# Kernel optimization log

Measured on AMD Instinct MI355X. Metric: run time of the kernel, lower is better.

The kernel has to match this reference:

```python
import jax, jax.numpy as jnp
import numpy as np

EPS = 1e-5

def _layernorm(h, g, b):
    m = jnp.mean(h, axis=-1, keepdims=True)
    v = jnp.mean((h - m) ** 2, axis=-1, keepdims=True)
    return (h - m) * jax.lax.rsqrt(v + EPS) * g + b

def setup_inputs() -> dict:
    B, N, D, H, C = 16, 4096, 1024, 512, 2
    key = jax.random.key(0)
    ks = jax.random.split(key, 16)
    def lin(k, fan_in, shape):
        return jax.random.normal(k, shape, dtype=jnp.float32) / np.sqrt(fan_in)
    return {
        "x":   jax.random.normal(ks[0], (B, N, D), dtype=jnp.float32),
        "W1":  lin(ks[1], D, (D, H)),  "b1": jnp.zeros((H,), jnp.float32),
        "g1":  jnp.ones((H,), jnp.float32), "beta1": jnp.zeros((H,), jnp.float32),
        "W2":  lin(ks[2], H, (H, H)),  "b2": jnp.zeros((H,), jnp.float32),
        "g2":  jnp.ones((H,), jnp.float32), "beta2": jnp.zeros((H,), jnp.float32),
        "Wa1": lin(ks[3], H, (H, H)),  "ba1": jnp.zeros((H,), jnp.float32),
        "wa2": lin(ks[4], H, (H, 1)),  "ba2": jnp.zeros((1,), jnp.float32),
        "Wc1": lin(ks[5], H, (H, H)),  "bc1": jnp.zeros((H,), jnp.float32),
        "Wc2": lin(ks[6], H, (H, C)),  "bc2": jnp.zeros((C,), jnp.float32),
    }

def reference(x, W1, b1, g1, beta1, W2, b2, g2, beta2,
              Wa1, ba1, wa2, ba2, Wc1, bc1, Wc2, bc2):
    # Feature extractor: Linear -> LayerNorm -> ReLU (x2); dropout is identity (eval)
    h = jax.nn.relu(_layernorm(jnp.einsum('bnd,dh->bnh', x, W1) + b1, g1, beta1))
    h = jax.nn.relu(_layernorm(jnp.einsum('bnh,hk->bnk', h, W2) + b2, g2, beta2))
    # Attention: Linear -> Tanh -> Linear(->1), softmax over instances (per bag)
    scores = jnp.tanh(jnp.einsum('bnh,hk->bnk', h, Wa1) + ba1) @ wa2 + ba2  # [B,N,1]
    attn = jax.nn.softmax(scores, axis=1)                                   # [B,N,1]
    pooled = jnp.sum(h * attn, axis=1)                                      # [B,H]
    # Classifier (no sample_source path): Linear -> ReLU -> Linear
    logits = jax.nn.relu(pooled @ Wc1 + bc1) @ Wc2 + bc2                    # [B,C]
    return logits
```

## Files before the change

### kernel.cpp

```cpp
#include <hip/hip_runtime.h>
#include <hip/hip_bf16.h>


#define MTOT   65536
#define DDIM   1024
#define HDIM   512
#define NBAG   16
#define NINST  4096

typedef __attribute__((ext_vector_type(8))) short bf16x8;
typedef __attribute__((ext_vector_type(4))) float f32x4;

__device__ __forceinline__ unsigned short f2bf(float f) {
  __hip_bfloat16 h = __float2bfloat16(f);
  unsigned short u;
  __builtin_memcpy(&u, &h, 2);
  return u;
}
__device__ __forceinline__ float bf2f(unsigned short u) {
  unsigned int x = ((unsigned int)u) << 16;
  float f;
  __builtin_memcpy(&f, &x, 4);
  return f;
}

__device__ __forceinline__ void gload16(const void* g, void* l) {
  __builtin_amdgcn_global_load_lds(
      (const __attribute__((address_space(1))) unsigned int*)g,
      (__attribute__((address_space(3))) unsigned int*)l, 16, 0, 0);
}

__device__ __forceinline__ bf16x8 pack8(float4 a, float4 b) {
  bf16x8 r;
  r[0] = (short)f2bf(a.x); r[1] = (short)f2bf(a.y);
  r[2] = (short)f2bf(a.z); r[3] = (short)f2bf(a.w);
  r[4] = (short)f2bf(b.x); r[5] = (short)f2bf(b.y);
  r[6] = (short)f2bf(b.z); r[7] = (short)f2bf(b.w);
  return r;
}

__global__ void transpose_cast(const float* __restrict__ src,
                               __hip_bfloat16* __restrict__ dst,
                               int R, int C) {
  __shared__ float t[32][33];
  const int c0 = blockIdx.x * 32, r0 = blockIdx.y * 32;
  const int tx = threadIdx.x, ty = threadIdx.y;
#pragma unroll
  for (int i = 0; i < 32; i += 8)
    t[ty + i][tx] = src[(size_t)(r0 + ty + i) * C + c0 + tx];
  __syncthreads();
#pragma unroll
  for (int i = 0; i < 32; i += 8)
    dst[(size_t)(c0 + ty + i) * R + r0 + tx] = __float2bfloat16(t[tx][ty + i]);
}

#define BM 128
#define BK 64
#define NW 8

template <int KD, bool AF32, int MODE>
__global__ __launch_bounds__(512, 2)
void gemm_fused(const void* Ap, const __hip_bfloat16* __restrict__ BT,
                const float* __restrict__ bias, const float* __restrict__ gg,
                const float* __restrict__ bb, const float* __restrict__ wa2,
                const float* __restrict__ ba2, __hip_bfloat16* __restrict__ outh,
                float* __restrict__ outs) {
  __shared__ __hip_bfloat16 At[2][BM * BK];
  __shared__ __hip_bfloat16 Bt[HDIM * BK];
  __shared__ float redS[BM][4];
  __shared__ float redQ[BM][4];
  __shared__ float muL[BM];
  __shared__ float rsL[BM];

  const int tid  = threadIdx.x;
  const int lane = tid & 63;
  const int w    = tid >> 6;
  const int wm   = w >> 2;
  const int wn   = w & 3;
  const int l16  = lane & 15;
  const int lg   = lane >> 4;
  const size_t row0 = (size_t)blockIdx.x * BM;

  const int sr = tid >> 3;
  const int sp = tid & 7;

  f32x4 acc[4][8];
#pragma unroll
  for (int i = 0; i < 4; i++)
#pragma unroll
    for (int j = 0; j < 8; j++) acc[i][j] = (f32x4){0.f, 0.f, 0.f, 0.f};

  const int NT = KD / BK;
  const __hip_bfloat16* Abf = (const __hip_bfloat16*)Ap;
  const float* Af32 = (const float*)Ap;

  auto stageB = [&](int kb) {
#pragma unroll
    for (int i = 0; i < 8; i++) {
      const int row = i * 64 + sr;
      const int slog = sp ^ (row & 7);
      gload16(BT + (size_t)row * KD + kb + slog * 8, &Bt[row * BK + sp * 8]);
    }
  };
  auto stageA_lds = [&](int kb, int buf) {
#pragma unroll
    for (int j = 0; j < 2; j++) {
      const int row = j * 64 + sr;
      const int slog = sp ^ (row & 7);
      gload16(Abf + (row0 + row) * KD + kb + slog * 8,
              &At[buf][row * BK + sp * 8]);
    }
  };

  float4 fa[2][2];
  auto loadA_f32 = [&](int kb) {
#pragma unroll
    for (int j = 0; j < 2; j++) {
      const int row = j * 64 + sr;
      const int slog = sp ^ (row & 7);
      const float* gp = Af32 + (row0 + row) * KD + kb + slog * 8;
      fa[j][0] = *reinterpret_cast<const float4*>(gp);
      fa[j][1] = *reinterpret_cast<const float4*>(gp + 4);
    }
  };
  auto writeA_f32 = [&](int buf) {
#pragma unroll
    for (int j = 0; j < 2; j++) {
      const int row = j * 64 + sr;
      *reinterpret_cast<bf16x8*>(&At[buf][row * BK + sp * 8]) =
          pack8(fa[j][0], fa[j][1]);
    }
  };

  if (AF32) {
    loadA_f32(0);
    writeA_f32(0);
  } else {
    stageA_lds(0, 0);
  }
  stageB(0);
  __syncthreads();

  int cur = 0;
  for (int t = 0; t < NT; ++t) {
    const int kb_next = (t + 1) * BK;
    if (t + 1 < NT) {
      if (AF32) loadA_f32(kb_next);
      else      stageA_lds(kb_next, cur ^ 1);
    }
#pragma unroll
    for (int h = 0; h < 2; ++h) {
      bf16x8 af[4], bfr[8];
#pragma unroll
      for (int fm = 0; fm < 4; fm++) {
        const int row = wm * 64 + fm * 16 + l16;
        const int s = (h * 4 + lg) ^ (row & 7);
        af[fm] = *reinterpret_cast<const bf16x8*>(&At[cur][row * BK + s * 8]);
      }
#pragma unroll
      for (int fn = 0; fn < 8; fn++) {
        const int row = wn * 128 + fn * 16 + l16;
        const int s = (h * 4 + lg) ^ (row & 7);
        bfr[fn] = *reinterpret_cast<const bf16x8*>(&Bt[row * BK + s * 8]);
      }
#pragma unroll
      for (int fm = 0; fm < 4; fm++)
#pragma unroll
        for (int fn = 0; fn < 8; fn++)
          acc[fm][fn] = __builtin_amdgcn_mfma_f32_16x16x32_bf16(
              af[fm], bfr[fn], acc[fm][fn], 0, 0, 0);
    }
    __syncthreads();
    if (t + 1 < NT) {
      if (AF32) writeA_f32(cur ^ 1);
      stageB(kb_next);
    }
    __syncthreads();
    cur ^= 1;
  }

  float biasv[8];
#pragma unroll
  for (int fn = 0; fn < 8; fn++) biasv[fn] = bias[wn * 128 + fn * 16 + l16];

  if (MODE == 0) {
    float gv[8], bv[8];
#pragma unroll
    for (int fn = 0; fn < 8; fn++) {
      const int col = wn * 128 + fn * 16 + l16;
      gv[fn] = gg[col];
      bv[fn] = bb[col];
    }
#pragma unroll
    for (int fm = 0; fm < 4; fm++)
#pragma unroll
      for (int r = 0; r < 4; r++) {
        float s1 = 0.f, s2 = 0.f;
#pragma unroll
        for (int fn = 0; fn < 8; fn++) {
          const float v = acc[fm][fn][r] + biasv[fn];
          s1 += v;
          s2 += v * v;
        }
#pragma unroll
        for (int m = 1; m < 16; m <<= 1) {
          s1 += __shfl_xor(s1, m);
          s2 += __shfl_xor(s2, m);
        }
        if (l16 == 0) {
          const int rl = wm * 64 + fm * 16 + lg * 4 + r;
          redS[rl][wn] = s1;
          redQ[rl][wn] = s2;
        }
      }
    __syncthreads();
    if (tid < BM) {
      const float S = redS[tid][0] + redS[tid][1] + redS[tid][2] + redS[tid][3];
      const float Q = redQ[tid][0] + redQ[tid][1] + redQ[tid][2] + redQ[tid][3];
      const float mean = S * (1.f / 512.f);
      const float var = Q * (1.f / 512.f) - mean * mean;
      muL[tid] = mean;
      rsL[tid] = rsqrtf(var + 1e-5f);
    }
    __syncthreads();
#pragma unroll
    for (int fm = 0; fm < 4; fm++)
#pragma unroll
      for (int r = 0; r < 4; r++) {
        const int rl = wm * 64 + fm * 16 + lg * 4 + r;
        const float mu = muL[rl], rs = rsL[rl];
#pragma unroll
        for (int fn = 0; fn < 8; fn++) {
          const float v = acc[fm][fn][r] + biasv[fn];
          float y = (v - mu) * rs * gv[fn] + bv[fn];
          y = fmaxf(y, 0.f);
          outh[(row0 + rl) * HDIM + wn * 128 + fn * 16 + l16] =
              __float2bfloat16(y);
        }
      }
  } else {
    float wv[8];
#pragma unroll
    for (int fn = 0; fn < 8; fn++) wv[fn] = wa2[wn * 128 + fn * 16 + l16];
#pragma unroll
    for (int fm = 0; fm < 4; fm++)
#pragma unroll
      for (int r = 0; r < 4; r++) {
        float s = 0.f;
#pragma unroll
        for (int fn = 0; fn < 8; fn++) {
          const float v = acc[fm][fn][r] + biasv[fn];
          s += tanhf(v) * wv[fn];
        }
#pragma unroll
        for (int m = 1; m < 16; m <<= 1) s += __shfl_xor(s, m);
        if (l16 == 0) redS[wm * 64 + fm * 16 + lg * 4 + r][wn] = s;
      }
    __syncthreads();
    if (tid < BM) {
      outs[row0 + tid] =
          redS[tid][0] + redS[tid][1] + redS[tid][2] + redS[tid][3] + ba2[0];
    }
  }
}

__global__ void softmax_bag(const float* __restrict__ sc, float* __restrict__ at) {
  const int b = blockIdx.x;
  const int tid = threadIdx.x;
  const int lane = tid & 63, w = tid >> 6;
  const float* s = sc + (size_t)b * NINST;
  float v[16];
  float mx = -1e30f;
#pragma unroll
  for (int i = 0; i < 16; i++) {
    v[i] = s[tid + i * 256];
    mx = fmaxf(mx, v[i]);
  }
#pragma unroll
  for (int off = 32; off; off >>= 1) mx = fmaxf(mx, __shfl_xor(mx, off));
  __shared__ float red[4];
  if (lane == 0) red[w] = mx;
  __syncthreads();
  mx = fmaxf(fmaxf(red[0], red[1]), fmaxf(red[2], red[3]));
  float sum = 0.f;
#pragma unroll
  for (int i = 0; i < 16; i++) {
    v[i] = expf(v[i] - mx);
    sum += v[i];
  }
#pragma unroll
  for (int off = 32; off; off >>= 1) sum += __shfl_xor(sum, off);
  __shared__ float red2[4];
  if (lane == 0) red2[w] = sum;
  __syncthreads();
  sum = red2[0] + red2[1] + red2[2] + red2[3];
  const float inv = 1.f / sum;
#pragma unroll
  for (int i = 0; i < 16; i++) at[(size_t)b * NINST + tid + i * 256] = v[i] * inv;
}

__global__ void pooled_partial(const __hip_bfloat16* __restrict__ h2,
                               const float* __restrict__ at,
                               float* __restrict__ part) {
  const int bid = blockIdx.x;
  const int b = bid >> 5, cc = (bid >> 3) & 3, nch = bid & 7;
  const int tid = threadIdx.x;
  const int c4 = (tid & 31) * 4, sub = tid >> 5;
  const int n0 = nch * 512;
  const size_t base = (size_t)b * NINST;
  float a0 = 0.f, a1 = 0.f, a2 = 0.f, a3 = 0.f;
  for (int n = n0 + sub; n < n0 + 512; n += 8) {
    const float a = at[base + n];
    const ushort4 u = *reinterpret_cast<const ushort4*>(
        &h2[(base + n) * HDIM + cc * 128 + c4]);
    a0 += a * bf2f(u.x);
    a1 += a * bf2f(u.y);
    a2 += a * bf2f(u.z);
    a3 += a * bf2f(u.w);
  }
  __shared__ float pb[8][128];
  pb[sub][c4 + 0] = a0;
  pb[sub][c4 + 1] = a1;
  pb[sub][c4 + 2] = a2;
  pb[sub][c4 + 3] = a3;
  __syncthreads();
  if (tid < 128) {
    float s = 0.f;
#pragma unroll
    for (int j = 0; j < 8; j++) s += pb[j][tid];
    part[(size_t)nch * 8192 + b * 512 + cc * 128 + tid] = s;
  }
}

__global__ void pooled_reduce(const float* __restrict__ part,
                              float* __restrict__ pooled) {
  const int i = blockIdx.x * 256 + threadIdx.x;
  float s = 0.f;
#pragma unroll
  for (int j = 0; j < 8; j++) s += part[(size_t)j * 8192 + i];
  pooled[i] = s;
}

__global__ void classifier(const float* __restrict__ pooled,
                           const float* __restrict__ Wc1,
                           const float* __restrict__ bc1,
                           const float* __restrict__ Wc2,
                           const float* __restrict__ bc2,
                           float* __restrict__ out) {
  __shared__ float P[NBAG][512];
  __shared__ float Rb[NBAG][512];
  const int tid = threadIdx.x;
#pragma unroll
  for (int i = 0; i < NBAG; i++) P[i][tid] = pooled[i * 512 + tid];
  __syncthreads();
  float r[NBAG];
#pragma unroll
  for (int i = 0; i < NBAG; i++) r[i] = 0.f;
  for (int k = 0; k < 512; k++) {
    const float wv = Wc1[k * 512 + tid];
#pragma unroll
    for (int i = 0; i < NBAG; i++) r[i] += P[i][k] * wv;
  }
#pragma unroll
  for (int i = 0; i < NBAG; i++) Rb[i][tid] = fmaxf(r[i] + bc1[tid], 0.f);
  __syncthreads();
  if (tid < 32) {
    const int i = tid >> 1, c = tid & 1;
    float s = bc2[c];
    for (int k = 0; k < 512; k++) s += Rb[i][k] * Wc2[k * 2 + c];
    out[i * 2 + c] = s;
  }
}

extern "C" void kernel_launch(void* const* d_in, const int* in_sizes, int n_in,
                              void* d_out, int out_size, void* d_ws,
                              size_t ws_size, hipStream_t stream) {
  const float* x   = (const float*)d_in[0];
  const float* W1  = (const float*)d_in[1];
  const float* b1  = (const float*)d_in[2];
  const float* g1  = (const float*)d_in[3];
  const float* be1 = (const float*)d_in[4];
  const float* W2  = (const float*)d_in[5];
  const float* b2  = (const float*)d_in[6];
  const float* g2  = (const float*)d_in[7];
  const float* be2 = (const float*)d_in[8];
  const float* Wa1 = (const float*)d_in[9];
  const float* ba1 = (const float*)d_in[10];
  const float* wa2 = (const float*)d_in[11];
  const float* ba2 = (const float*)d_in[12];
  const float* Wc1 = (const float*)d_in[13];
  const float* bc1 = (const float*)d_in[14];
  const float* Wc2 = (const float*)d_in[15];
  const float* bc2 = (const float*)d_in[16];
  float* out = (float*)d_out;

  char* ws = (char*)d_ws;
  __hip_bfloat16* W1T = (__hip_bfloat16*)(ws + 0);
  __hip_bfloat16* W2T = (__hip_bfloat16*)(ws + 1048576);
  __hip_bfloat16* WaT = (__hip_bfloat16*)(ws + 1572864);
  float* scores = (float*)(ws + 2097152);
  float* attn   = (float*)(ws + 2359296);
  float* part   = (float*)(ws + 2621440);
  float* pooled = (float*)(ws + 2883584);
  __hip_bfloat16* hbuf = (__hip_bfloat16*)(ws + 4194304);

  transpose_cast<<<dim3(16, 32), dim3(32, 8), 0, stream>>>(W1, W1T, DDIM, HDIM);
  transpose_cast<<<dim3(16, 16), dim3(32, 8), 0, stream>>>(W2, W2T, HDIM, HDIM);
  transpose_cast<<<dim3(16, 16), dim3(32, 8), 0, stream>>>(Wa1, WaT, HDIM, HDIM);

  gemm_fused<DDIM, true, 0><<<MTOT / BM, 512, 0, stream>>>(
      x, W1T, b1, g1, be1, nullptr, nullptr, hbuf, nullptr);
  gemm_fused<HDIM, false, 0><<<MTOT / BM, 512, 0, stream>>>(
      hbuf, W2T, b2, g2, be2, nullptr, nullptr, hbuf, nullptr);
  gemm_fused<HDIM, false, 1><<<MTOT / BM, 512, 0, stream>>>(
      hbuf, WaT, ba1, nullptr, nullptr, wa2, ba2, nullptr, scores);

  softmax_bag<<<NBAG, 256, 0, stream>>>(scores, attn);
  pooled_partial<<<512, 256, 0, stream>>>(hbuf, attn, part);
  pooled_reduce<<<32, 256, 0, stream>>>(part, pooled);
  classifier<<<1, 512, 0, stream>>>(pooled, Wc1, bc1, Wc2, bc2, out);
}
```

Baseline: 386.5 us.

## Deepen GEMM main loop into multi-stage async pipeline with split MFMA phases

Reworks the fused GEMM main loop to use BK=32 with a 4-deep B buffer ring and double-buffered A, issuing global loads two steps ahead. Explicit vmcnt/lgkmcnt waits, split-phase barriers, sched_barrier and setprio interleave the loads with two halves of the MFMA work. The goal is to hide global and LDS load latency behind tensor-core math instead of stalling on a full __syncthreads each k-step. In exchange it adds more barriers per k-step and fragile hand-counted waitcnt values, which could cause races or stalls if the counts are wrong.

```diff
diff --git a/kernel.cpp b/kernel.cpp
--- a/kernel.cpp
+++ b/kernel.cpp
@@ -39,6 +39,9 @@
   return r;
 }
 
+#define VMW(N) asm volatile("s_waitcnt vmcnt(" #N ")" ::: "memory")
+#define LKW0   asm volatile("s_waitcnt lgkmcnt(0)" ::: "memory")
+
 __global__ void transpose_cast(const float* __restrict__ src,
                                __hip_bfloat16* __restrict__ dst,
                                int R, int C) {
@@ -55,8 +58,7 @@
 }
 
 #define BM 128
-#define BK 64
-#define NW 8
+#define BK 32
 
 template <int KD, bool AF32, int MODE>
 __global__ __launch_bounds__(512, 2)
@@ -66,7 +68,7 @@
                 const float* __restrict__ ba2, __hip_bfloat16* __restrict__ outh,
                 float* __restrict__ outs) {
   __shared__ __hip_bfloat16 At[2][BM * BK];
-  __shared__ __hip_bfloat16 Bt[HDIM * BK];
+  __shared__ __hip_bfloat16 Bt[4][HDIM * BK];
   __shared__ float redS[BM][4];
   __shared__ float redQ[BM][4];
   __shared__ float muL[BM];
@@ -81,103 +83,123 @@
   const int lg   = lane >> 4;
   const size_t row0 = (size_t)blockIdx.x * BM;
 
-  const int sr = tid >> 3;
-  const int sp = tid & 7;
-
-  f32x4 acc[4][8];
-#pragma unroll
-  for (int i = 0; i < 4; i++)
-#pragma unroll
-    for (int j = 0; j < 8; j++) acc[i][j] = (f32x4){0.f, 0.f, 0.f, 0.f};
-
-  const int NT = KD / BK;
+  const int sr = tid >> 2;
+  const int sp = tid & 3;
+  const int slogA = sp ^ (sr & 3);
+
+  constexpr int NT = KD / BK;
   const __hip_bfloat16* Abf = (const __hip_bfloat16*)Ap;
   const float* Af32 = (const float*)Ap;
 
-  auto stageB = [&](int kb) {
-#pragma unroll
-    for (int i = 0; i < 8; i++) {
-      const int row = i * 64 + sr;
-      const int slog = sp ^ (row & 7);
-      gload16(BT + (size_t)row * KD + kb + slog * 8, &Bt[row * BK + sp * 8]);
+  f32x4 acc[4][8];
+#pragma unroll
+  for (int i = 0; i < 4; i++)
+#pragma unroll
+    for (int j = 0; j < 8; j++) acc[i][j] = (f32x4){0.f, 0.f, 0.f, 0.f};
+
+  auto issueB2 = [&](int kb, int buf, int half) {
+#pragma unroll
+    for (int i = 0; i < 2; i++) {
+      const int row = (half * 2 + i) * 128 + sr;
+      const int slog = sp ^ (row & 3);
+      gload16(BT + (size_t)row * KD + kb + slog * 8, &Bt[buf][row * BK + sp * 8]);
     }
   };
-  auto stageA_lds = [&](int kb, int buf) {
-#pragma unroll
-    for (int j = 0; j < 2; j++) {
-      const int row = j * 64 + sr;
-      const int slog = sp ^ (row & 7);
-      gload16(Abf + (row0 + row) * KD + kb + slog * 8,
-              &At[buf][row * BK + sp * 8]);
-    }
+  auto issueA_g = [&](int kb, int buf) {
+    gload16(Abf + (row0 + sr) * KD + kb + slogA * 8, &At[buf][sr * BK + sp * 8]);
   };
 
-  float4 fa[2][2];
-  auto loadA_f32 = [&](int kb) {
-#pragma unroll
-    for (int j = 0; j < 2; j++) {
-      const int row = j * 64 + sr;
-      const int slog = sp ^ (row & 7);
-      const float* gp = Af32 + (row0 + row) * KD + kb + slog * 8;
-      fa[j][0] = *reinterpret_cast<const float4*>(gp);
-      fa[j][1] = *reinterpret_cast<const float4*>(gp + 4);
-    }
-  };
-  auto writeA_f32 = [&](int buf) {
-#pragma unroll
-    for (int j = 0; j < 2; j++) {
-      const int row = j * 64 + sr;
-      *reinterpret_cast<bf16x8*>(&At[buf][row * BK + sp * 8]) =
-          pack8(fa[j][0], fa[j][1]);
-    }
-  };
-
-  if (AF32) {
-    loadA_f32(0);
-    writeA_f32(0);
+  float4 fr0a, fr0b, fr1a, fr1b;
+#define LOADA(FR, TT)                                                          \
+  { const float* gp_ = Af32 + (row0 + sr) * KD + (TT) * BK + slogA * 8;        \
+    FR##a = *reinterpret_cast<const float4*>(gp_);                             \
+    FR##b = *reinterpret_cast<const float4*>(gp_ + 4); }
+#define CVTA(FR, BUF)                                                          \
+  { *reinterpret_cast<bf16x8*>(&At[(BUF)][sr * BK + sp * 8]) =                 \
+        pack8(FR##a, FR##b); }
+
+#define MFMA_HALF(FN0)                                                         \
+  _Pragma("unroll") for (int fm = 0; fm < 4; fm++)                             \
+  _Pragma("unroll") for (int fn = (FN0); fn < (FN0) + 4; fn++)                 \
+      acc[fm][fn] = __builtin_amdgcn_mfma_f32_16x16x32_bf16(                   \
+          af[fm], bfr[fn], acc[fm][fn], 0, 0, 0);
+
+  if constexpr (AF32) {
+    LOADA(fr0, 0); VMW(0); CVTA(fr0, 0);
+    issueB2(0, 0, 0); issueB2(0, 0, 1);
+    LOADA(fr1, 1);
+    issueB2(BK, 1, 0); issueB2(BK, 1, 1);
+    LKW0;
+    __builtin_amdgcn_s_barrier();
   } else {
-    stageA_lds(0, 0);
-  }
-  stageB(0);
-  __syncthreads();
-
-  int cur = 0;
-  for (int t = 0; t < NT; ++t) {
-    const int kb_next = (t + 1) * BK;
-    if (t + 1 < NT) {
-      if (AF32) loadA_f32(kb_next);
-      else      stageA_lds(kb_next, cur ^ 1);
-    }
-#pragma unroll
-    for (int h = 0; h < 2; ++h) {
-      bf16x8 af[4], bfr[8];
-#pragma unroll
-      for (int fm = 0; fm < 4; fm++) {
-        const int row = wm * 64 + fm * 16 + l16;
-        const int s = (h * 4 + lg) ^ (row & 7);
-        af[fm] = *reinterpret_cast<const bf16x8*>(&At[cur][row * BK + s * 8]);
-      }
-#pragma unroll
-      for (int fn = 0; fn < 8; fn++) {
-        const int row = wn * 128 + fn * 16 + l16;
-        const int s = (h * 4 + lg) ^ (row & 7);
-        bfr[fn] = *reinterpret_cast<const bf16x8*>(&Bt[row * BK + s * 8]);
-      }
-#pragma unroll
-      for (int fm = 0; fm < 4; fm++)
-#pragma unroll
-        for (int fn = 0; fn < 8; fn++)
-          acc[fm][fn] = __builtin_amdgcn_mfma_f32_16x16x32_bf16(
-              af[fm], bfr[fn], acc[fm][fn], 0, 0, 0);
-    }
-    __syncthreads();
-    if (t + 1 < NT) {
-      if (AF32) writeA_f32(cur ^ 1);
-      stageB(kb_next);
-    }
-    __syncthreads();
-    cur ^= 1;
-  }
+    issueA_g(0, 0);
+    issueB2(0, 0, 0); issueB2(0, 0, 1);
+    issueB2(BK, 1, 0); issueB2(BK, 1, 1);
+    __builtin_amdgcn_s_barrier();
+  }
+
+#define GSTEP(J)                                                               \
+  {                                                                            \
+    const int t = tb + (J);                                                    \
+    if constexpr (AF32) { VMW(6); } else { VMW(4); }                           \
+    bf16x8 af[4], bfr[8];                                                      \
+    _Pragma("unroll") for (int fm = 0; fm < 4; fm++) {                         \
+      const int row = wm * 64 + fm * 16 + l16;                                 \
+      af[fm] = *reinterpret_cast<const bf16x8*>(                               \
+          &At[(J) & 1][row * BK + (lg ^ (row & 3)) * 8]);                      \
+    }                                                                          \
+    _Pragma("unroll") for (int fn = 0; fn < 4; fn++) {                         \
+      const int row = wn * 128 + fn * 16 + l16;                                \
+      bfr[fn] = *reinterpret_cast<const bf16x8*>(                              \
+          &Bt[(J) & 3][row * BK + (lg ^ (row & 3)) * 8]);                      \
+    }                                                                          \
+    if constexpr (AF32) {                                                      \
+      if (t + 2 < NT) {                                                        \
+        if constexpr (((J) & 1) == 0) { LOADA(fr0, t + 2); }                   \
+        else                          { LOADA(fr1, t + 2); }                   \
+      }                                                                        \
+    } else {                                                                   \
+      if (t + 1 < NT) issueA_g((t + 1) * BK, ((J) + 1) & 1);                   \
+    }                                                                          \
+    if (t + 2 < NT) issueB2((t + 2) * BK, ((J) + 2) & 3, 0);                   \
+    __builtin_amdgcn_s_barrier();                                              \
+    LKW0; __builtin_amdgcn_sched_barrier(0);                                   \
+    __builtin_amdgcn_s_setprio(1);                                             \
+    MFMA_HALF(0)                                                               \
+    __builtin_amdgcn_s_setprio(0);                                             \
+    __builtin_amdgcn_s_barrier();                                              \
+    _Pragma("unroll") for (int fn = 4; fn < 8; fn++) {                         \
+      const int row = wn * 128 + fn * 16 + l16;                                \
+      bfr[fn] = *reinterpret_cast<const bf16x8*>(                              \
+          &Bt[(J) & 3][row * BK + (lg ^ (row & 3)) * 8]);                      \
+    }                                                                          \
+    if (t + 2 < NT) issueB2((t + 2) * BK, ((J) + 2) & 3, 1);                   \
+    if constexpr (AF32) {                                                      \
+      if (t + 1 < NT) {                                                        \
+        VMW(10);                                                               \
+        if constexpr (((J) & 1) == 0) { CVTA(fr1, ((J) + 1) & 1); }            \
+        else                          { CVTA(fr0, ((J) + 1) & 1); }            \
+        LKW0;                                                                  \
+      }                                                                        \
+    }                                                                          \
+    __builtin_amdgcn_s_barrier();                                              \
+    LKW0; __builtin_amdgcn_sched_barrier(0);                                   \
+    __builtin_amdgcn_s_setprio(1);                                             \
+    MFMA_HALF(4)                                                               \
+    __builtin_amdgcn_s_setprio(0);                                             \
+    __builtin_amdgcn_s_barrier();                                              \
+  }
+
+  for (int tb = 0; tb < NT; tb += 4) {
+    GSTEP(0)
+    GSTEP(1)
+    GSTEP(2)
+    GSTEP(3)
+  }
+#undef GSTEP
+#undef LOADA
+#undef CVTA
+#undef MFMA_HALF
 
   float biasv[8];
 #pragma unroll
```

Result: no change. 390.6 us (+1.1%).
